# Kernel optimization log

Hardware: AMD Instinct MI355X
Metric: run time of the kernel (lower is better)

The kernel has to match this reference:

```python
import jax, jax.numpy as jnp
import numpy as np

LN_EPS = 1e-5

def layer_norm(x, w, b):
    mu = jnp.mean(x, axis=-1, keepdims=True)
    var = jnp.var(x, axis=-1, keepdims=True)
    return (x - mu) * jax.lax.rsqrt(var + LN_EPS) * w + b

def masked_softmax_topk(ctx, k):
    # ctx: [B, D, D]; keep top-k per row (scatter-style mask), softmax over last dim
    B, D, _ = ctx.shape
    idx = jax.lax.top_k(ctx, k)[1]                       # [B, D, k]
    mask = jnp.zeros(ctx.shape, bool).at[
        jnp.arange(B)[:, None, None], jnp.arange(D)[None, :, None], idx
    ].set(True)
    return jax.nn.softmax(jnp.where(mask, ctx, -jnp.inf), axis=-1)

def setup_inputs() -> dict:
    key = jax.random.key(0)
    ks = jax.random.split(key, 8)
    B, H, W, C = 8, 96, 96, 256
    x1 = jax.random.normal(ks[0], (B, H, W, C), jnp.float32)
    x2 = jax.random.normal(ks[1], (B, H, W, C), jnp.float32)
    norm1_w = jnp.ones((C,), jnp.float32)
    norm1_b = jnp.zeros((C,), jnp.float32)
    reproj_w = jax.random.normal(ks[2], (2 * C, C), jnp.float32) * (1.0 / np.sqrt(C))  # 1x1 conv
    reproj_b = jnp.zeros((2 * C,), jnp.float32)
    norm2_w = jnp.ones((2 * C,), jnp.float32)
    norm2_b = jnp.zeros((2 * C,), jnp.float32)
    attn_w = jnp.full((4,), 0.25, jnp.float32)  # attn1..attn4 scalars
    return {"x1": x1, "x2": x2, "norm1_w": norm1_w, "norm1_b": norm1_b,
            "reproj_w": reproj_w, "reproj_b": reproj_b,
            "norm2_w": norm2_w, "norm2_b": norm2_b, "attn_w": attn_w}

def reference(x1, x2, norm1_w, norm1_b, reproj_w, reproj_b, norm2_w, norm2_b, attn_w):
    B, H, W, C = x1.shape
    N, D = H * W, C  # head_count = 1
    n1 = layer_norm(x1.reshape(B, N, C), norm1_w, norm1_b)   # values source
    n2 = layer_norm(x2.reshape(B, N, C), norm1_w, norm1_b)   # keys/queries source
    kq = jnp.swapaxes(n2, 1, 2)                              # [B, D, N]
    values = jnp.swapaxes(n1, 1, 2)                          # [B, D, N]
    keyv = jax.nn.softmax(kq, axis=2)                        # softmax over N
    query = jax.nn.softmax(kq, axis=1)                       # softmax over channels
    context = jnp.einsum('bdn,ben->bde', keyv, values)       # [B, D, D]
    ks = [D // 2, (D * 2) // 3, (D * 3) // 4, (D * 4) // 5]
    attended = jnp.zeros((B, D, N), x1.dtype)
    for i, k in enumerate(ks):
        attn = masked_softmax_topk(context, k)               # [B, D, D]
        attended = attended + attn_w[i] * jnp.einsum('bde,ben->bdn', attn, query)
    # 1x1 conv reprojection D -> 2D, then LayerNorm over 2D
    rp = jnp.einsum('od,bdn->bno', reproj_w, attended) + reproj_b  # [B, N, 2D]
    rp = layer_norm(rp, norm2_w, norm2_b)
    out = rp.reshape(B, H, W, 2 * C).transpose(0, 3, 1, 2)   # [B, 2C, H, W]
    return out
```

## Files before the change

kernel.cpp:

```cpp
#include <hip/hip_runtime.h>
#include <math.h>

typedef __attribute__((ext_vector_type(8))) short short8;
typedef __attribute__((ext_vector_type(4))) float f32x4;
typedef unsigned short u16;
typedef unsigned int u32;

constexpr int Bb = 8;
constexpr int Nn = 9216;
constexpr int Cc = 256;
constexpr int Oo = 512;
constexpr float LN_EPS = 1e-5f;
constexpr int KS2 = 16;

static __device__ __forceinline__ u16 f2bf(float f) {
    unsigned u = __builtin_bit_cast(unsigned, f);
    u += 0x7fffu + ((u >> 16) & 1u);
    return (u16)(u >> 16);
}
static __device__ __forceinline__ float bf2f(u16 u) {
    return __builtin_bit_cast(float, (unsigned)u << 16);
}

__global__ __launch_bounds__(512, 2) void k_pre(const float* __restrict__ x2,
                                                const float* __restrict__ x1,
                                                const float* __restrict__ lnw,
                                                const float* __restrict__ lnb,
                                                u16* __restrict__ Kexp,
                                                u16* __restrict__ V,
                                                float* __restrict__ rowsum,
                                                float* __restrict__ pS) {
    __shared__ float wsh[256], bsh[256];
    __shared__ float wred[8][256];
    const int b = blockIdx.z;
    const int doExp = (blockIdx.y == 0);
    const float* src = doExp ? x2 : x1;
    u16* dst = doExp ? Kexp : V;
    const int nc = (blockIdx.x & 7) * 18 + (blockIdx.x >> 3);
    const int n0 = nc * 64;
    const int t = threadIdx.x;
    if (t < 256) { wsh[t] = lnw[t]; bsh[t] = lnb[t]; }
    __syncthreads();

    const int r = t >> 3;
    const int g = t & 7;
    const int wv = t >> 6;
    const long long row = (long long)b * Nn + n0 + r;
    const float* rowp = src + row * Cc;

    float4 v[8];
#pragma unroll
    for (int i = 0; i < 8; ++i)
        v[i] = *reinterpret_cast<const float4*>(rowp + g * 4 + i * 32);

    float s = 0.f, q = 0.f;
#pragma unroll
    for (int i = 0; i < 8; ++i) {
        s += v[i].x + v[i].y + v[i].z + v[i].w;
        q += v[i].x * v[i].x + v[i].y * v[i].y + v[i].z * v[i].z + v[i].w * v[i].w;
    }
    s += __shfl_xor(s, 1); s += __shfl_xor(s, 2); s += __shfl_xor(s, 4);
    q += __shfl_xor(q, 1); q += __shfl_xor(q, 2); q += __shfl_xor(q, 4);
    const float mu = s * (1.0f / Cc);
    const float rstd = rsqrtf(q * (1.0f / Cc) - mu * mu + LN_EPS);

    float se = 0.f;
    u16 h[8][4];
#pragma unroll
    for (int i = 0; i < 8; ++i) {
        const int d = g * 4 + i * 32;
        const float4 w4 = *reinterpret_cast<const float4*>(&wsh[d]);
        const float4 b4 = *reinterpret_cast<const float4*>(&bsh[d]);
        v[i].x = (v[i].x - mu) * rstd * w4.x + b4.x;
        v[i].y = (v[i].y - mu) * rstd * w4.y + b4.y;
        v[i].z = (v[i].z - mu) * rstd * w4.z + b4.z;
        v[i].w = (v[i].w - mu) * rstd * w4.w + b4.w;
        if (doExp) {
            v[i].x = __expf(v[i].x); v[i].y = __expf(v[i].y);
            v[i].z = __expf(v[i].z); v[i].w = __expf(v[i].w);
            se += v[i].x + v[i].y + v[i].z + v[i].w;
        }
        h[i][0] = f2bf(v[i].x); h[i][1] = f2bf(v[i].y);
        h[i][2] = f2bf(v[i].z); h[i][3] = f2bf(v[i].w);
        int2 pk;
        pk.x = (int)((unsigned)h[i][0] | ((unsigned)h[i][1] << 16));
        pk.y = (int)((unsigned)h[i][2] | ((unsigned)h[i][3] << 16));
        *reinterpret_cast<int2*>(dst + row * Cc + d) = pk;
    }

    if (doExp) {
        se += __shfl_xor(se, 1); se += __shfl_xor(se, 2); se += __shfl_xor(se, 4);
        if (g == 0) rowsum[row] = se;
#pragma unroll
        for (int i = 0; i < 8; ++i) {
            float c0 = bf2f(h[i][0]), c1 = bf2f(h[i][1]);
            float c2 = bf2f(h[i][2]), c3 = bf2f(h[i][3]);
#pragma unroll
            for (int m = 8; m <= 32; m <<= 1) {
                c0 += __shfl_xor(c0, m); c1 += __shfl_xor(c1, m);
                c2 += __shfl_xor(c2, m); c3 += __shfl_xor(c3, m);
            }
            if ((t & 63) < 8) {
                const int d = g * 4 + i * 32;
                wred[wv][d + 0] = c0; wred[wv][d + 1] = c1;
                wred[wv][d + 2] = c2; wred[wv][d + 3] = c3;
            }
        }
        __syncthreads();
        if (t < 256) {
            float ss = 0.f;
#pragma unroll
            for (int i = 0; i < 8; ++i) ss += wred[i][t];
            pS[((long long)b * 144 + nc) * Cc + t] = ss;
        }
    }
}

__global__ __launch_bounds__(256) void k_ctx2(const u16* __restrict__ Kexp,
                                              const u16* __restrict__ V,
                                              float* __restrict__ ctxp) {
    __shared__ alignas(16) unsigned char smemRaw[32768];
    u16* Asm = reinterpret_cast<u16*>(smemRaw);
    u16* Bsm = reinterpret_cast<u16*>(smemRaw + 16384);
    float (*patch)[16][68] = reinterpret_cast<float (*)[16][68]>(smemRaw);

    const int t = threadIdx.x;
    const int b = blockIdx.z, kc = blockIdx.y;
    const int d0 = (blockIdx.x >> 1) * 128, e0 = (blockIdx.x & 1) * 128;
    const int l = t & 63, w = t >> 6;
    const int wr = w >> 1, wc = w & 1;
    const int frow = l & 15, fk = (l >> 4) << 3;
    const int sr = t & 63, sw = t >> 6;

    f32x4 acc[4][4] = {};

    for (int kt = 0; kt < 9; ++kt) {
        const long long nb = (long long)b * Nn + kc * 576 + kt * 64;
        int4 av[4], bv[4];
#pragma unroll
        for (int j = 0; j < 4; ++j) {
            const int c8 = sw * 4 + j;
            av[j] = *reinterpret_cast<const int4*>(Kexp + (nb + sr) * Cc + d0 + c8 * 8);
            bv[j] = *reinterpret_cast<const int4*>(V + (nb + sr) * Cc + e0 + c8 * 8);
        }
        __syncthreads();
#pragma unroll
        for (int j = 0; j < 4; ++j) {
            const u16* pa = reinterpret_cast<const u16*>(&av[j]);
            const u16* pb = reinterpret_cast<const u16*>(&bv[j]);
#pragma unroll
            for (int e8 = 0; e8 < 8; ++e8) {
                const int dd = (sw * 4 + j) * 8 + e8;
                const int col = sr ^ (e8 << 3);
                Asm[dd * 64 + col] = pa[e8];
                Bsm[dd * 64 + col] = pb[e8];
            }
        }
        __syncthreads();
#pragma unroll
        for (int kf = 0; kf < 2; ++kf) {
            short8 af[4], bf[4];
            const int kk = kf * 32 + fk;
#pragma unroll
            for (int mi = 0; mi < 4; ++mi) {
                const int rw_ = wr * 64 + mi * 16 + frow;
                af[mi] = *reinterpret_cast<const short8*>(&Asm[rw_ * 64 + (kk ^ ((rw_ & 7) << 3))]);
            }
#pragma unroll
            for (int ni = 0; ni < 4; ++ni) {
                const int rw_ = wc * 64 + ni * 16 + frow;
                bf[ni] = *reinterpret_cast<const short8*>(&Bsm[rw_ * 64 + (kk ^ ((rw_ & 7) << 3))]);
            }
#pragma unroll
            for (int mi = 0; mi < 4; ++mi)
#pragma unroll
                for (int ni = 0; ni < 4; ++ni)
                    acc[mi][ni] = __builtin_amdgcn_mfma_f32_16x16x32_bf16(af[mi], bf[ni], acc[mi][ni], 0, 0, 0);
        }
    }

    __syncthreads();
    float* Cg = ctxp + ((long long)kc * Bb + b) * Cc * Cc;
    const int crow0 = (l >> 4) * 4, ccol = l & 15;
#pragma unroll
    for (int mi = 0; mi < 4; ++mi) {
#pragma unroll
        for (int ni = 0; ni < 4; ++ni)
#pragma unroll
            for (int r_ = 0; r_ < 4; ++r_)
                patch[w][crow0 + r_][ni * 16 + ccol] = acc[mi][ni][r_];
        asm volatile("s_waitcnt lgkmcnt(0)" ::: "memory");
        __builtin_amdgcn_sched_barrier(0);
#pragma unroll
        for (int row = 0; row < 16; ++row)
            Cg[(long long)(d0 + wr * 64 + mi * 16 + row) * Cc + e0 + wc * 64 + l] = patch[w][row][l];
        asm volatile("s_waitcnt lgkmcnt(0)" ::: "memory");
        __builtin_amdgcn_sched_barrier(0);
    }
}

__global__ __launch_bounds__(256) void k_rankred(const float* __restrict__ ctxp,
                                                 const float* __restrict__ pS,
                                                 const float* __restrict__ aw,
                                                 float* __restrict__ Ac) {
    __shared__ float row[256];
    __shared__ float red[256];
    const int d = blockIdx.x, b = blockIdx.y, e = threadIdx.x;

    red[e] = (e < 144) ? pS[((long long)b * 144 + e) * Cc + d] : 0.f;
    __syncthreads();
    for (int s_ = 128; s_; s_ >>= 1) { if (e < s_) red[e] += red[e + s_]; __syncthreads(); }
    const float invCol = 1.0f / red[0];
    __syncthreads();

    float c = 0.f;
#pragma unroll
    for (int kc = 0; kc < KS2; ++kc)
        c += ctxp[(((long long)kc * Bb + b) * Cc + d) * Cc + e];
    c *= invCol;
    row[e] = c;
    __syncthreads();
    int p = 0;
    for (int j = 0; j < 256; ++j) {
        const float cj = row[j];
        p += (cj > c) || (cj == c && j < e);
    }
    red[e] = c; __syncthreads();
    for (int s_ = 128; s_; s_ >>= 1) { if (e < s_) red[e] = fmaxf(red[e], red[e + s_]); __syncthreads(); }
    const float m = red[0];
    const float ex = __expf(c - m);
    const int kks[4] = {128, 170, 192, 204};
    float Zv[4];
#pragma unroll
    for (int i = 0; i < 4; ++i) {
        __syncthreads();
        red[e] = (p < kks[i]) ? ex : 0.0f;
        __syncthreads();
        for (int s_ = 128; s_; s_ >>= 1) { if (e < s_) red[e] += red[e + s_]; __syncthreads(); }
        Zv[i] = red[0];
    }
    float wsum = 0.0f;
#pragma unroll
    for (int i = 0; i < 4; ++i)
        if (p < kks[i]) wsum += aw[i] / Zv[i];
    Ac[((long long)(b * Cc + d)) * Cc + e] = ex * wsum;
}

__global__ __launch_bounds__(256) void k_wa(const float* __restrict__ W,
                                            const float* __restrict__ Ac,
                                            u16* __restrict__ WAb16) {
    __shared__ float As[16][64], Bs[16][64];
    const int b = blockIdx.y;
    const int o0 = (blockIdx.x >> 2) * 64, e0 = (blockIdx.x & 3) * 64;
    const int t = threadIdx.x, tx = t & 15, ty = t >> 4;
    const int a_oo = t >> 2, a_k4 = (t & 3) * 4;
    const int b_kk = t >> 4, b_e4 = (t & 15) * 4;
    float acc[4][4] = {{0.f}};
    for (int kd = 0; kd < 256; kd += 16) {
        const float4 wv = *reinterpret_cast<const float4*>(W + (o0 + a_oo) * Cc + kd + a_k4);
        const float4 av = *reinterpret_cast<const float4*>(Ac + ((long long)(b * Cc + kd + b_kk)) * Cc + e0 + b_e4);
        __syncthreads();
        As[a_k4 + 0][a_oo] = wv.x; As[a_k4 + 1][a_oo] = wv.y;
        As[a_k4 + 2][a_oo] = wv.z; As[a_k4 + 3][a_oo] = wv.w;
        *reinterpret_cast<float4*>(&Bs[b_kk][b_e4]) = av;
        __syncthreads();
#pragma unroll
        for (int kk = 0; kk < 16; ++kk) {
            const float4 a4 = *reinterpret_cast<const float4*>(&As[kk][ty * 4]);
            const float4 b4 = *reinterpret_cast<const float4*>(&Bs[kk][tx * 4]);
            const float aa[4] = {a4.x, a4.y, a4.z, a4.w};
            const float bb[4] = {b4.x, b4.y, b4.z, b4.w};
#pragma unroll
            for (int i = 0; i < 4; ++i)
#pragma unroll
                for (int j = 0; j < 4; ++j) acc[i][j] = fmaf(aa[i], bb[j], acc[i][j]);
        }
    }
#pragma unroll
    for (int i = 0; i < 4; ++i) {
        int2 pk;
        pk.x = (int)((unsigned)f2bf(acc[i][0]) | ((unsigned)f2bf(acc[i][1]) << 16));
        pk.y = (int)((unsigned)f2bf(acc[i][2]) | ((unsigned)f2bf(acc[i][3]) << 16));
        *reinterpret_cast<int2*>(WAb16 + ((long long)(b * Oo + o0 + ty * 4 + i)) * Cc + e0 + tx * 4) = pk;
    }
}

__global__ __launch_bounds__(256, 3) void k_rpln(const u16* __restrict__ Kexp,
                                                 const float* __restrict__ rowsum,
                                                 const u16* __restrict__ WAb16,
                                                 const float* __restrict__ rbias,
                                                 const float* __restrict__ nw,
                                                 const float* __restrict__ nb,
                                                 float* __restrict__ out) {
    __shared__ float patch[4][16][36];
    __shared__ float psum[32][4], psq[32][4];
    __shared__ float muA[32], rsA[32];
    __shared__ float irow[32];

    const int t = threadIdx.x;
    const int b = blockIdx.z;
    const int nt_ = (blockIdx.x & 7) * 36 + (blockIdx.x >> 3);
    const int n0 = nt_ * 32;
    const int l = t & 63, w = t >> 6;
    const int frow = l & 15, fk = (l >> 4) << 3;
    const int hi = l >> 4;

    if (t < 32) irow[t] = 1.0f / rowsum[(long long)b * Nn + n0 + t];

    f32x4 acc[2][8] = {};

    const u16* Aq = Kexp + ((long long)b * Nn + n0) * Cc;
    const u16* Bw = WAb16 + ((long long)b * Oo + w * 128) * Cc;

    int4 aF[2][8];
#pragma unroll
    for (int mi = 0; mi < 2; ++mi)
#pragma unroll
        for (int s = 0; s < 8; ++s)
            aF[mi][s] = *reinterpret_cast<const int4*>(Aq + (mi * 16 + frow) * Cc + s * 32 + fk);

    int4 bC[8], bN[8];
#pragma unroll
    for (int ni = 0; ni < 8; ++ni)
        bC[ni] = *reinterpret_cast<const int4*>(Bw + (ni * 16 + frow) * Cc + fk);

#pragma unroll
    for (int s = 0; s < 8; ++s) {
        if (s < 7) {
            const int kk = (s + 1) * 32 + fk;
#pragma unroll
            for (int ni = 0; ni < 8; ++ni)
                bN[ni] = *reinterpret_cast<const int4*>(Bw + (ni * 16 + frow) * Cc + kk);
        }
#pragma unroll
        for (int mi = 0; mi < 2; ++mi)
#pragma unroll
            for (int ni = 0; ni < 8; ++ni)
                acc[mi][ni] = __builtin_amdgcn_mfma_f32_16x16x32_bf16(
                    __builtin_bit_cast(short8, aF[mi][s]), __builtin_bit_cast(short8, bC[ni]),
                    acc[mi][ni], 0, 0, 0);
        if (s < 7) {
#pragma unroll
            for (int ni = 0; ni < 8; ++ni) bC[ni] = bN[ni];
        }
    }

    __syncthreads();
#pragma unroll
    for (int ni = 0; ni < 8; ++ni) {
        const float bb = rbias[w * 128 + ni * 16 + frow];
#pragma unroll
        for (int mi = 0; mi < 2; ++mi)
#pragma unroll
            for (int r_ = 0; r_ < 4; ++r_) {
                const int rw_ = mi * 16 + hi * 4 + r_;
                acc[mi][ni][r_] = acc[mi][ni][r_] * irow[rw_] + bb;
            }
    }
#pragma unroll
    for (int mi = 0; mi < 2; ++mi)
#pragma unroll
        for (int r_ = 0; r_ < 4; ++r_) {
            float s = 0.f, q = 0.f;
#pragma unroll
            for (int ni = 0; ni < 8; ++ni) { const float v = acc[mi][ni][r_]; s += v; q += v * v; }
#pragma unroll
            for (int m = 8; m; m >>= 1) { s += __shfl_xor(s, m); q += __shfl_xor(q, m); }
            if (frow == 0) {
                const int row = mi * 16 + hi * 4 + r_;
                psum[row][w] = s; psq[row][w] = q;
            }
        }
    __syncthreads();
    if (t < 32) {
        const float s = psum[t][0] + psum[t][1] + psum[t][2] + psum[t][3];
        const float q = psq[t][0] + psq[t][1] + psq[t][2] + psq[t][3];
        const float m = s * (1.0f / Oo);
        muA[t] = m;
        rsA[t] = rsqrtf(q * (1.0f / Oo) - m * m + LN_EPS);
    }
    __syncthreads();

    float nwv[8], nbv[8];
#pragma unroll
    for (int ni = 0; ni < 8; ++ni) {
        const int o = w * 128 + ni * 16 + frow;
        nwv[ni] = nw[o]; nbv[ni] = nb[o];
    }

#pragma unroll
    for (int ni = 0; ni < 8; ++ni) {
#pragma unroll
        for (int mi = 0; mi < 2; ++mi)
#pragma unroll
            for (int r_ = 0; r_ < 4; ++r_) {
                const int nl = mi * 16 + hi * 4 + r_;
                patch[w][frow][nl] = (acc[mi][ni][r_] - muA[nl]) * rsA[nl] * nwv[ni] + nbv[ni];
            }
        asm volatile("s_waitcnt lgkmcnt(0)" ::: "memory");
        __builtin_amdgcn_sched_barrier(0);
#pragma unroll
        for (int p = 0; p < 2; ++p) {
            const int o_loc = p * 8 + (l >> 3);
            const int colf4 = l & 7;
            const f32x4 v = *reinterpret_cast<const f32x4*>(&patch[w][o_loc][colf4 * 4]);
            const int o_g = w * 128 + ni * 16 + o_loc;
            __builtin_nontemporal_store(v,
                reinterpret_cast<f32x4*>(&out[((long long)(b * Oo + o_g)) * Nn + n0 + colf4 * 4]));
        }
        asm volatile("s_waitcnt lgkmcnt(0)" ::: "memory");
        __builtin_amdgcn_sched_barrier(0);
    }
}

extern "C" void kernel_launch(void* const* d_in, const int* in_sizes, int n_in,
                              void* d_out, int out_size, void* d_ws, size_t ws_size,
                              hipStream_t stream) {
    (void)in_sizes; (void)n_in; (void)out_size; (void)ws_size;
    const float* x1    = (const float*)d_in[0];
    const float* x2    = (const float*)d_in[1];
    const float* n1w   = (const float*)d_in[2];
    const float* n1b   = (const float*)d_in[3];
    const float* rw    = (const float*)d_in[4];
    const float* rbias = (const float*)d_in[5];
    const float* n2w   = (const float*)d_in[6];
    const float* n2b   = (const float*)d_in[7];
    const float* aw    = (const float*)d_in[8];
    float* out = (float*)d_out;

    u16* V = (u16*)d_out;

    float* ws = (float*)d_ws;
    size_t off = 0;
    u16*   Kexp   = (u16*)(ws + off); off += (size_t)Bb * Nn * Cc / 2;
    float* ctxp   = ws + off; off += (size_t)KS2 * Bb * Cc * Cc;
    float* Ac     = ws + off; off += (size_t)Bb * Cc * Cc;
    u16*   WAb16  = (u16*)(ws + off); off += (size_t)Bb * Oo * Cc / 2;
    float* pS     = ws + off; off += (size_t)Bb * 144 * Cc;
    float* rowsum = ws + off; off += (size_t)Bb * Nn;

    k_pre<<<dim3(144, 2, Bb), 512, 0, stream>>>(x2, x1, n1w, n1b, Kexp, V, rowsum, pS);
    k_ctx2<<<dim3(4, KS2, Bb), 256, 0, stream>>>(Kexp, V, ctxp);
    k_rankred<<<dim3(Cc, Bb), 256, 0, stream>>>(ctxp, pS, aw, Ac);
    k_wa<<<dim3(32, Bb), 256, 0, stream>>>(rw, Ac, WAb16);
    k_rpln<<<dim3(288, 1, Bb), 256, 0, stream>>>(Kexp, rowsum, WAb16, rbias, n2w, n2b, out);
}
```

Measured before the change: 223.4 us.

## Double row tile in reprojection+LayerNorm kernel to 64 rows with 8 waves

The final GEMM+LayerNorm kernel now processes 64 spatial rows per block using 512 threads arranged as 2x4 waves, instead of 32 rows with 4 waves. Output stores become 256-byte contiguous runs per output channel instead of 128-byte, improving write coalescing, and the grid halves. In exchange the per-ni patch staging now needs block-wide __syncthreads instead of wave-local waits, and launch_bounds(512,3) may pressure registers.

```diff
diff --git a/kernel.cpp b/kernel.cpp
--- a/kernel.cpp
+++ b/kernel.cpp
@@ -285,32 +285,33 @@
     }
 }
 
-__global__ __launch_bounds__(256, 3) void k_rpln(const u16* __restrict__ Kexp,
+__global__ __launch_bounds__(512, 3) void k_rpln(const u16* __restrict__ Kexp,
                                                  const float* __restrict__ rowsum,
                                                  const u16* __restrict__ WAb16,
                                                  const float* __restrict__ rbias,
                                                  const float* __restrict__ nw,
                                                  const float* __restrict__ nb,
                                                  float* __restrict__ out) {
-    __shared__ float patch[4][16][36];
-    __shared__ float psum[32][4], psq[32][4];
-    __shared__ float muA[32], rsA[32];
-    __shared__ float irow[32];
+    __shared__ float patch[4][16][66];
+    __shared__ float psum[64][4], psq[64][4];
+    __shared__ float muA[64], rsA[64];
+    __shared__ float irow[64];
 
     const int t = threadIdx.x;
     const int b = blockIdx.z;
-    const int nt_ = (blockIdx.x & 7) * 36 + (blockIdx.x >> 3);
-    const int n0 = nt_ * 32;
+    const int nt_ = (blockIdx.x & 7) * 18 + (blockIdx.x >> 3);
+    const int n0 = nt_ * 64;
     const int l = t & 63, w = t >> 6;
+    const int wr = w >> 2, wc = w & 3;
     const int frow = l & 15, fk = (l >> 4) << 3;
     const int hi = l >> 4;
 
-    if (t < 32) irow[t] = 1.0f / rowsum[(long long)b * Nn + n0 + t];
+    if (t < 64) irow[t] = 1.0f / rowsum[(long long)b * Nn + n0 + t];
 
     f32x4 acc[2][8] = {};
 
-    const u16* Aq = Kexp + ((long long)b * Nn + n0) * Cc;
-    const u16* Bw = WAb16 + ((long long)b * Oo + w * 128) * Cc;
+    const u16* Aq = Kexp + ((long long)b * Nn + n0 + wr * 32) * Cc;
+    const u16* Bw = WAb16 + ((long long)b * Oo + wc * 128) * Cc;
 
     int4 aF[2][8];
 #pragma unroll
@@ -348,12 +349,12 @@
     __syncthreads();
 #pragma unroll
     for (int ni = 0; ni < 8; ++ni) {
-        const float bb = rbias[w * 128 + ni * 16 + frow];
+        const float bb = rbias[wc * 128 + ni * 16 + frow];
 #pragma unroll
         for (int mi = 0; mi < 2; ++mi)
 #pragma unroll
             for (int r_ = 0; r_ < 4; ++r_) {
-                const int rw_ = mi * 16 + hi * 4 + r_;
+                const int rw_ = wr * 32 + mi * 16 + hi * 4 + r_;
                 acc[mi][ni][r_] = acc[mi][ni][r_] * irow[rw_] + bb;
             }
     }
@@ -367,12 +368,12 @@
 #pragma unroll
             for (int m = 8; m; m >>= 1) { s += __shfl_xor(s, m); q += __shfl_xor(q, m); }
             if (frow == 0) {
-                const int row = mi * 16 + hi * 4 + r_;
-                psum[row][w] = s; psq[row][w] = q;
-            }
-        }
-    __syncthreads();
-    if (t < 32) {
+                const int row = wr * 32 + mi * 16 + hi * 4 + r_;
+                psum[row][wc] = s; psq[row][wc] = q;
+            }
+        }
+    __syncthreads();
+    if (t < 64) {
         const float s = psum[t][0] + psum[t][1] + psum[t][2] + psum[t][3];
         const float q = psq[t][0] + psq[t][1] + psq[t][2] + psq[t][3];
         const float m = s * (1.0f / Oo);
@@ -384,7 +385,7 @@
     float nwv[8], nbv[8];
 #pragma unroll
     for (int ni = 0; ni < 8; ++ni) {
-        const int o = w * 128 + ni * 16 + frow;
+        const int o = wc * 128 + ni * 16 + frow;
         nwv[ni] = nw[o]; nbv[ni] = nb[o];
     }
 
@@ -394,22 +395,20 @@
         for (int mi = 0; mi < 2; ++mi)
 #pragma unroll
             for (int r_ = 0; r_ < 4; ++r_) {
-                const int nl = mi * 16 + hi * 4 + r_;
-                patch[w][frow][nl] = (acc[mi][ni][r_] - muA[nl]) * rsA[nl] * nwv[ni] + nbv[ni];
-            }
-        asm volatile("s_waitcnt lgkmcnt(0)" ::: "memory");
-        __builtin_amdgcn_sched_barrier(0);
+                const int nl = wr * 32 + mi * 16 + hi * 4 + r_;
+                patch[wc][frow][nl] = (acc[mi][ni][r_] - muA[nl]) * rsA[nl] * nwv[ni] + nbv[ni];
+            }
+        __syncthreads();
 #pragma unroll
         for (int p = 0; p < 2; ++p) {
-            const int o_loc = p * 8 + (l >> 3);
-            const int colf4 = l & 7;
-            const f32x4 v = *reinterpret_cast<const f32x4*>(&patch[w][o_loc][colf4 * 4]);
-            const int o_g = w * 128 + ni * 16 + o_loc;
+            const int o_loc = wr * 8 + p * 4 + hi;
+            const int colf4 = l & 15;
+            const f32x4 v = *reinterpret_cast<const f32x4*>(&patch[wc][o_loc][colf4 * 4]);
+            const int o_g = wc * 128 + ni * 16 + o_loc;
             __builtin_nontemporal_store(v,
                 reinterpret_cast<f32x4*>(&out[((long long)(b * Oo + o_g)) * Nn + n0 + colf4 * 4]));
         }
-        asm volatile("s_waitcnt lgkmcnt(0)" ::: "memory");
-        __builtin_amdgcn_sched_barrier(0);
+        __syncthreads();
     }
 }
 
@@ -443,5 +442,5 @@
     k_ctx2<<<dim3(4, KS2, Bb), 256, 0, stream>>>(Kexp, V, ctxp);
     k_rankred<<<dim3(Cc, Bb), 256, 0, stream>>>(ctxp, pS, aw, Ac);
     k_wa<<<dim3(32, Bb), 256, 0, stream>>>(rw, Ac, WAb16);
-    k_rpln<<<dim3(288, 1, Bb), 256, 0, stream>>>(Kexp, rowsum, WAb16, rbias, n2w, n2b, out);
-}
+    k_rpln<<<dim3(144, 1, Bb), 512, 0, stream>>>(Kexp, rowsum, WAb16, rbias, n2w, n2b, out);
+}
```

Measured after the change: 256.1 us. +14.7%, slower.
